# Kernel optimization log

Hardware: AMD Instinct MI355X
Metric: run time of the kernel (lower is better)

The kernel has to match this reference:

```python
import jax, jax.numpy as jnp
import numpy as np

N, E = 50000, 800000
DIM_IN, DIM_H, DIM_OUT, HEADS = 128, 16, 64, 8
NEG_SLOPE = 0.2  # PyG GATv2Conv default


def setup_inputs() -> dict:
    key = jax.random.key(0)
    ks = jax.random.split(key, 10)
    s = 0.1
    x = jax.random.normal(ks[0], (N, DIM_IN), jnp.float32)
    edge_index = jax.random.randint(ks[1], (2, E), 0, N, dtype=jnp.int32)
    Wl1 = jax.random.normal(ks[2], (DIM_IN, HEADS * DIM_H), jnp.float32) * s
    Wr1 = jax.random.normal(ks[3], (DIM_IN, HEADS * DIM_H), jnp.float32) * s
    att1 = jax.random.normal(ks[4], (HEADS, DIM_H), jnp.float32) * s
    b1 = jnp.zeros((HEADS * DIM_H,), jnp.float32)
    Wl2 = jax.random.normal(ks[5], (HEADS * DIM_H, DIM_OUT), jnp.float32) * s
    Wr2 = jax.random.normal(ks[6], (HEADS * DIM_H, DIM_OUT), jnp.float32) * s
    att2 = jax.random.normal(ks[7], (1, DIM_OUT), jnp.float32) * s
    b2 = jnp.zeros((DIM_OUT,), jnp.float32)
    return dict(x=x, edge_index=edge_index, Wl1=Wl1, Wr1=Wr1, att1=att1, b1=b1,
                Wl2=Wl2, Wr2=Wr2, att2=att2, b2=b2)


def gatv2_conv(x, src, dst, Wl, Wr, att, bias, heads, out_ch):
    # PyG GATv2Conv (share_weights=False, concat=True)
    n = x.shape[0]
    xl = (x @ Wl).reshape(n, heads, out_ch)  # source-side transform
    xr = (x @ Wr).reshape(n, heads, out_ch)  # target-side transform
    e = jax.nn.leaky_relu(xl[src] + xr[dst], NEG_SLOPE)          # [E, H, C]
    logits = jnp.einsum('ehc,hc->eh', e, att)                    # [E, H]
    # segment softmax over incoming edges of each dst node
    m = jax.lax.stop_gradient(jax.ops.segment_max(logits, dst, num_segments=n))
    ex = jnp.exp(logits - m[dst])
    denom = jax.ops.segment_sum(ex, dst, num_segments=n)
    alpha = ex / denom[dst]                                      # [E, H]
    out = jax.ops.segment_sum(xl[src] * alpha[..., None], dst, num_segments=n)
    return out.reshape(n, heads * out_ch) + bias


def reference(x, edge_index, Wl1, Wr1, att1, b1, Wl2, Wr2, att2, b2):
    n = x.shape[0]
    loops = jnp.arange(n, dtype=edge_index.dtype)
    src = jnp.concatenate([edge_index[0], loops])  # add_self_loops=True
    dst = jnp.concatenate([edge_index[1], loops])
    h = gatv2_conv(x, src, dst, Wl1, Wr1, att1, b1, HEADS, DIM_H)
    h = jax.nn.elu(h)
    out = gatv2_conv(h, src, dst, Wl2, Wr2, att2, b2, 1, DIM_OUT)
    return jax.nn.log_softmax(out, axis=1)
```

## Files before the change

kernel.cpp:

```cpp
#include <hip/hip_runtime.h>
#include <cstdint>

#define DIM_IN 128
#define HEADS 8
#define DIM_H 16
#define H1 128
#define DIM_OUT 64
#define NEG 0.2f
#define CAP 6144

typedef __attribute__((ext_vector_type(8))) short bf16x8;
typedef __attribute__((ext_vector_type(4))) float f32x4;

__device__ __forceinline__ float blo(uint32_t u) { return __uint_as_float(u << 16); }
__device__ __forceinline__ float bhi(uint32_t u) { return __uint_as_float(u & 0xffff0000u); }
__device__ __forceinline__ unsigned short f2b(float f) {
  uint32_t u = __float_as_uint(f);
  u += 0x7fffu + ((u >> 16) & 1u);
  return (unsigned short)(u >> 16);
}

#define KP 0.86561702453337804f
#define KM 0.57707801635558536f

__global__ __launch_bounds__(256) void prep_fused(
    const float* __restrict__ x, unsigned short* __restrict__ xb, int totx,
    const float* __restrict__ W0, const float* __restrict__ W1,
    const float* __restrict__ W2, const float* __restrict__ W3,
    unsigned short* __restrict__ T0, unsigned short* __restrict__ T1,
    unsigned short* __restrict__ T2, unsigned short* __restrict__ T3,
    int xblocks) {
  int bx = blockIdx.x;
  if (bx < xblocks) {
    int i = (bx * 256 + threadIdx.x) * 8;
    if (i >= totx) return;
    float4 a = *(const float4*)(x + i);
    float4 b = *(const float4*)(x + i + 4);
    ushort4 u0 = {f2b(a.x), f2b(a.y), f2b(a.z), f2b(a.w)};
    ushort4 u1 = {f2b(b.x), f2b(b.y), f2b(b.z), f2b(b.w)};
    *(ushort4*)(xb + i) = u0;
    *(ushort4*)(xb + i + 4) = u1;
  } else {
    int wz = bx - xblocks;
    int z = wz >> 6;
    const float* W = (z == 0) ? W0 : (z == 1) ? W1 : (z == 2) ? W2 : W3;
    unsigned short* T = (z == 0) ? T0 : (z == 1) ? T1 : (z == 2) ? T2 : T3;
    int M = (z < 2) ? 128 : 64;
    int t = (wz & 63) * 256 + threadIdx.x;
    if (t >= M * 128) return;
    int n = t >> 7, k = t & 127;
    T[t] = f2b(W[k * M + n]);
  }
}

template <int M>
__global__ __launch_bounds__(256) void gemm_mfma(
    const unsigned short* __restrict__ A,
    const unsigned short* __restrict__ Bt0, const unsigned short* __restrict__ Bt1,
    unsigned short* __restrict__ C0, unsigned short* __restrict__ C1, int Nrows) {
  constexpr int K = 128;
  constexpr int LDA = 72;
  constexpr int MT = M / 2;
  constexpr int NT = MT / 16;
  __shared__ __align__(16) short Asm[128 * LDA];
  __shared__ __align__(16) short Bsm[M * LDA];
  const unsigned short* __restrict__ Bt = blockIdx.z ? Bt1 : Bt0;
  unsigned short* __restrict__ Cb = blockIdx.z ? C1 : C0;
  const int row0 = blockIdx.x * 128;
  const int tid = threadIdx.x;
  const int w = tid >> 6, lane = tid & 63;
  const int l = lane & 15, q = lane >> 4;
  const int wrow = (w >> 1) * 64, wcol = (w & 1) * MT;

  f32x4 zero = {0.f, 0.f, 0.f, 0.f};
  f32x4 acc[4][NT];
#pragma unroll
  for (int ti = 0; ti < 4; ++ti)
#pragma unroll
    for (int tj = 0; tj < NT; ++tj) acc[ti][tj] = zero;

  for (int k0 = 0; k0 < K; k0 += 64) {
    __syncthreads();
    {
      int r = tid >> 1, sg = (tid & 1) * 32;
      int grow = row0 + r;
      const uint4* src = (const uint4*)(A + (size_t)grow * K + k0 + sg);
      uint4 z4 = make_uint4(0, 0, 0, 0);
#pragma unroll
      for (int i = 0; i < 4; ++i) {
        uint4 v = (grow < Nrows) ? src[i] : z4;
        *(uint4*)(Asm + r * LDA + sg + i * 8) = v;
      }
    }
    {
      int r = tid >> 1, sg = (tid & 1) * 32;
      if (r < M) {
        const uint4* src = (const uint4*)(Bt + (size_t)r * K + k0 + sg);
#pragma unroll
        for (int i = 0; i < 4; ++i)
          *(uint4*)(Bsm + r * LDA + sg + i * 8) = src[i];
      }
    }
    __syncthreads();
#pragma unroll
    for (int kk = 0; kk < 64; kk += 32) {
      bf16x8 af[4], bfr[NT];
#pragma unroll
      for (int ti = 0; ti < 4; ++ti)
        af[ti] = *(const bf16x8*)(Asm + (wrow + ti * 16 + l) * LDA + kk + q * 8);
#pragma unroll
      for (int tj = 0; tj < NT; ++tj)
        bfr[tj] = *(const bf16x8*)(Bsm + (wcol + tj * 16 + l) * LDA + kk + q * 8);
#pragma unroll
      for (int ti = 0; ti < 4; ++ti)
#pragma unroll
        for (int tj = 0; tj < NT; ++tj)
          acc[ti][tj] = __builtin_amdgcn_mfma_f32_16x16x32_bf16(
              af[ti], bfr[tj], acc[ti][tj], 0, 0, 0);
    }
  }
#pragma unroll
  for (int ti = 0; ti < 4; ++ti) {
#pragma unroll
    for (int tj = 0; tj < NT; ++tj) {
      int col = wcol + tj * 16 + l;
#pragma unroll
      for (int r = 0; r < 4; ++r) {
        int grow = row0 + wrow + ti * 16 + q * 4 + r;
        if (grow < Nrows) Cb[(size_t)grow * M + col] = f2b(acc[ti][tj][r]);
      }
    }
  }
}

__global__ __launch_bounds__(256) void p1_bucket(
    const int* __restrict__ ei, int* __restrict__ gcnt,
    uint32_t* __restrict__ gbuf, int E, int nbkt) {
  __shared__ int hist[256];
  __shared__ int base[256];
  __shared__ int cur[256];
  int tid = threadIdx.x;
  hist[tid] = 0;
  __syncthreads();
  int e0 = blockIdx.x * 8192;
  int nE = min(8192, E - e0);
  for (int i = tid; i < nE; i += 256)
    atomicAdd(&hist[ei[E + e0 + i] >> 8], 1);
  __syncthreads();
  if (tid < nbkt) {
    int h = hist[tid];
    base[tid] = h ? atomicAdd(&gcnt[tid], h) : 0;
  }
  cur[tid] = 0;
  __syncthreads();
  for (int i = tid; i < nE; i += 256) {
    int d = ei[E + e0 + i];
    int s = ei[e0 + i];
    int b = d >> 8;
    int r = atomicAdd(&cur[b], 1);
    int pos = base[b] + r;
    if (pos < CAP) gbuf[(size_t)b * CAP + pos] = ((uint32_t)d << 16) | (uint32_t)s;
  }
}

__device__ __forceinline__ int block_excl_scan256(int v, int* tmp) {
  int lane = threadIdx.x & 63, wid = threadIdx.x >> 6;
  int x = v;
#pragma unroll
  for (int o = 1; o < 64; o <<= 1) {
    int y = __shfl_up(x, o, 64);
    if (lane >= o) x += y;
  }
  if (lane == 63) tmp[wid] = x;
  __syncthreads();
  int prefix = 0;
#pragma unroll
  for (int w = 0; w < 4; ++w) if (w < wid) prefix += tmp[w];
  __syncthreads();
  return prefix + x - v;
}

__global__ __launch_bounds__(256) void p2_fused(
    const uint32_t* __restrict__ gbuf, const int* __restrict__ gcnt,
    int* __restrict__ off, int* __restrict__ srcs, int N, int nbkt) {
  __shared__ int sb[256];
  __shared__ int hist[256];
  __shared__ int cur[256];
  __shared__ int tmp[4];
  int b = blockIdx.x, tid = threadIdx.x;
  int gv = (tid < nbkt) ? gcnt[tid] : 0;
  int gex = block_excl_scan256(gv, tmp);
  sb[tid] = gex;
  hist[tid] = 0;
  __syncthreads();
  int base = sb[b];
  int cnt = min(gcnt[b], CAP);
  const uint32_t* p = gbuf + (size_t)b * CAP;
  for (int i = tid; i < cnt; i += 256)
    atomicAdd(&hist[(p[i] >> 16) & 255], 1);
  __syncthreads();
  int d = hist[tid];
  int excl = block_excl_scan256(d, tmp);
  int idx = (b << 8) + tid;
  int o = base + excl;
  if (idx <= N) off[idx] = o;
  cur[tid] = o;
  __syncthreads();
  for (int i = tid; i < cnt; i += 256) {
    uint32_t v = p[i];
    int pos = atomicAdd(&cur[(v >> 16) & 255], 1);
    srcs[pos] = (int)(v & 0xFFFFu);
  }
}

__global__ __launch_bounds__(256) void agg_l1(
    const int* __restrict__ srcs, const int* __restrict__ off,
    const unsigned short* __restrict__ xlb, const unsigned short* __restrict__ xrb,
    const float* __restrict__ att, const float* __restrict__ b1,
    unsigned short* __restrict__ hbb, int N) {
  int wid = threadIdx.x >> 6, lane = threadIdx.x & 63;
  int node = blockIdx.x * 4 + wid;
  if (node >= N) return;
  const int l4 = lane & 15;
  const int g  = lane >> 4;
  uint4 xru = *(const uint4*)(xrb + ((size_t)node << 7) + (l4 << 3));
  float r0 = blo(xru.x), r1 = bhi(xru.x), r2 = blo(xru.y), r3 = bhi(xru.y);
  float r4 = blo(xru.z), r5 = bhi(xru.z), r6 = blo(xru.w), r7 = bhi(xru.w);
  float4 a0  = *(const float4*)(att + (l4 << 3));
  float4 a1  = *(const float4*)(att + (l4 << 3) + 4);
  float c0 = KP * a0.x, c1 = KP * a0.y, c2 = KP * a0.z, c3 = KP * a0.w;
  float c4 = KP * a1.x, c5 = KP * a1.y, c6 = KP * a1.z, c7 = KP * a1.w;
  float d0 = KM * a0.x, d1 = KM * a0.y, d2 = KM * a0.z, d3 = KM * a0.w;
  float d4 = KM * a1.x, d5 = KM * a1.y, d6 = KM * a1.z, d7 = KM * a1.w;
  float acc0 = 0.f, acc1 = 0.f, acc2 = 0.f, acc3 = 0.f;
  float acc4 = 0.f, acc5 = 0.f, acc6 = 0.f, acc7 = 0.f;
  float dsum = 0.f;
  int beg = off[node];
  int M = off[node + 1] - beg + 1;
  for (int base = 0; base < M; base += 64) {
    int nk = min(64, M - base);
    int v = base + lane;
    int sv = 0;
    if (lane < nk) sv = (v == 0) ? node : srcs[beg + v - 1];
    int niter = (nk + 3) >> 2;
    for (int it = 0; it < niter; ++it) {
      int j = (it << 2) + g;
      int s = __shfl(sv, j, 64);
      uint4 xu = *(const uint4*)(xlb + ((size_t)s << 7) + (l4 << 3));
      float x0 = blo(xu.x), x1 = bhi(xu.x), x2 = blo(xu.y), x3 = bhi(xu.y);
      float x4 = blo(xu.z), x5 = bhi(xu.z), x6 = blo(xu.w), x7 = bhi(xu.w);
      float t, p;
      t = x0 + r0; p = fmaf(d0, fabsf(t), c0 * t);
      t = x1 + r1; p = fmaf(c1, t, p); p = fmaf(d1, fabsf(t), p);
      t = x2 + r2; p = fmaf(c2, t, p); p = fmaf(d2, fabsf(t), p);
      t = x3 + r3; p = fmaf(c3, t, p); p = fmaf(d3, fabsf(t), p);
      t = x4 + r4; p = fmaf(c4, t, p); p = fmaf(d4, fabsf(t), p);
      t = x5 + r5; p = fmaf(c5, t, p); p = fmaf(d5, fabsf(t), p);
      t = x6 + r6; p = fmaf(c6, t, p); p = fmaf(d6, fabsf(t), p);
      t = x7 + r7; p = fmaf(c7, t, p); p = fmaf(d7, fabsf(t), p);
      p += __shfl_xor(p, 1, 64);
      float ev = (j < nk) ? __builtin_amdgcn_exp2f(p) : 0.f;
      acc0 = fmaf(ev, x0, acc0); acc1 = fmaf(ev, x1, acc1);
      acc2 = fmaf(ev, x2, acc2); acc3 = fmaf(ev, x3, acc3);
      acc4 = fmaf(ev, x4, acc4); acc5 = fmaf(ev, x5, acc5);
      acc6 = fmaf(ev, x6, acc6); acc7 = fmaf(ev, x7, acc7);
      dsum += ev;
    }
  }
#pragma unroll
  for (int o = 16; o <= 32; o <<= 1) {
    dsum += __shfl_xor(dsum, o, 64);
    acc0 += __shfl_xor(acc0, o, 64); acc1 += __shfl_xor(acc1, o, 64);
    acc2 += __shfl_xor(acc2, o, 64); acc3 += __shfl_xor(acc3, o, 64);
    acc4 += __shfl_xor(acc4, o, 64); acc5 += __shfl_xor(acc5, o, 64);
    acc6 += __shfl_xor(acc6, o, 64); acc7 += __shfl_xor(acc7, o, 64);
  }
  if (g == 0) {
    float inv = 1.0f / dsum;
    float4 bv0 = *(const float4*)(b1 + (l4 << 3));
    float4 bv1 = *(const float4*)(b1 + (l4 << 3) + 4);
    float o0 = fmaf(acc0, inv, bv0.x), o1 = fmaf(acc1, inv, bv0.y);
    float o2 = fmaf(acc2, inv, bv0.z), o3 = fmaf(acc3, inv, bv0.w);
    float o4 = fmaf(acc4, inv, bv1.x), o5 = fmaf(acc5, inv, bv1.y);
    float o6 = fmaf(acc6, inv, bv1.z), o7 = fmaf(acc7, inv, bv1.w);
    o0 = o0 > 0.f ? o0 : expm1f(o0); o1 = o1 > 0.f ? o1 : expm1f(o1);
    o2 = o2 > 0.f ? o2 : expm1f(o2); o3 = o3 > 0.f ? o3 : expm1f(o3);
    o4 = o4 > 0.f ? o4 : expm1f(o4); o5 = o5 > 0.f ? o5 : expm1f(o5);
    o6 = o6 > 0.f ? o6 : expm1f(o6); o7 = o7 > 0.f ? o7 : expm1f(o7);
    ushort4 h0 = {f2b(o0), f2b(o1), f2b(o2), f2b(o3)};
    ushort4 h1 = {f2b(o4), f2b(o5), f2b(o6), f2b(o7)};
    unsigned short* ph = hbb + ((size_t)node << 7) + (l4 << 3);
    *(ushort4*)(ph)     = h0;
    *(ushort4*)(ph + 4) = h1;
  }
}

__global__ __launch_bounds__(256) void agg_l2(
    const int* __restrict__ srcs, const int* __restrict__ off,
    const unsigned short* __restrict__ xlb, const unsigned short* __restrict__ xrb,
    const float* __restrict__ att, const float* __restrict__ b2,
    float* __restrict__ out, int N) {
  int wid = threadIdx.x >> 6, lane = threadIdx.x & 63;
  int node = blockIdx.x * 4 + wid;
  if (node >= N) return;
  const int l3 = lane & 7;
  const int g  = lane >> 3;
  uint4 xru = *(const uint4*)(xrb + ((size_t)node << 6) + (l3 << 3));
  float r0 = blo(xru.x), r1 = bhi(xru.x), r2 = blo(xru.y), r3 = bhi(xru.y);
  float r4 = blo(xru.z), r5 = bhi(xru.z), r6 = blo(xru.w), r7 = bhi(xru.w);
  float4 a0  = *(const float4*)(att + (l3 << 3));
  float4 a1  = *(const float4*)(att + (l3 << 3) + 4);
  float c0 = KP * a0.x, c1 = KP * a0.y, c2 = KP * a0.z, c3 = KP * a0.w;
  float c4 = KP * a1.x, c5 = KP * a1.y, c6 = KP * a1.z, c7 = KP * a1.w;
  float d0 = KM * a0.x, d1 = KM * a0.y, d2 = KM * a0.z, d3 = KM * a0.w;
  float d4 = KM * a1.x, d5 = KM * a1.y, d6 = KM * a1.z, d7 = KM * a1.w;
  float acc0 = 0.f, acc1 = 0.f, acc2 = 0.f, acc3 = 0.f;
  float acc4 = 0.f, acc5 = 0.f, acc6 = 0.f, acc7 = 0.f;
  float dsum = 0.f;
  int beg = off[node];
  int M = off[node + 1] - beg + 1;
  for (int base = 0; base < M; base += 64) {
    int nk = min(64, M - base);
    int v = base + lane;
    int sv = 0;
    if (lane < nk) sv = (v == 0) ? node : srcs[beg + v - 1];
    int niter = (nk + 7) >> 3;
    for (int it = 0; it < niter; ++it) {
      int j = (it << 3) + g;
      int s = __shfl(sv, j, 64);
      uint4 xu = *(const uint4*)(xlb + ((size_t)s << 6) + (l3 << 3));
      float x0 = blo(xu.x), x1 = bhi(xu.x), x2 = blo(xu.y), x3 = bhi(xu.y);
      float x4 = blo(xu.z), x5 = bhi(xu.z), x6 = blo(xu.w), x7 = bhi(xu.w);
      float t, p;
      t = x0 + r0; p = fmaf(d0, fabsf(t), c0 * t);
      t = x1 + r1; p = fmaf(c1, t, p); p = fmaf(d1, fabsf(t), p);
      t = x2 + r2; p = fmaf(c2, t, p); p = fmaf(d2, fabsf(t), p);
      t = x3 + r3; p = fmaf(c3, t, p); p = fmaf(d3, fabsf(t), p);
      t = x4 + r4; p = fmaf(c4, t, p); p = fmaf(d4, fabsf(t), p);
      t = x5 + r5; p = fmaf(c5, t, p); p = fmaf(d5, fabsf(t), p);
      t = x6 + r6; p = fmaf(c6, t, p); p = fmaf(d6, fabsf(t), p);
      t = x7 + r7; p = fmaf(c7, t, p); p = fmaf(d7, fabsf(t), p);
      p += __shfl_xor(p, 1, 64);
      p += __shfl_xor(p, 2, 64);
      p += __shfl_xor(p, 4, 64);
      float ev = (j < nk) ? __builtin_amdgcn_exp2f(p) : 0.f;
      acc0 = fmaf(ev, x0, acc0); acc1 = fmaf(ev, x1, acc1);
      acc2 = fmaf(ev, x2, acc2); acc3 = fmaf(ev, x3, acc3);
      acc4 = fmaf(ev, x4, acc4); acc5 = fmaf(ev, x5, acc5);
      acc6 = fmaf(ev, x6, acc6); acc7 = fmaf(ev, x7, acc7);
      dsum += ev;
    }
  }
#pragma unroll
  for (int o = 8; o <= 32; o <<= 1) {
    dsum += __shfl_xor(dsum, o, 64);
    acc0 += __shfl_xor(acc0, o, 64); acc1 += __shfl_xor(acc1, o, 64);
    acc2 += __shfl_xor(acc2, o, 64); acc3 += __shfl_xor(acc3, o, 64);
    acc4 += __shfl_xor(acc4, o, 64); acc5 += __shfl_xor(acc5, o, 64);
    acc6 += __shfl_xor(acc6, o, 64); acc7 += __shfl_xor(acc7, o, 64);
  }
  float inv = 1.0f / dsum;
  float4 bv0 = *(const float4*)(b2 + (l3 << 3));
  float4 bv1 = *(const float4*)(b2 + (l3 << 3) + 4);
  float v0 = fmaf(acc0, inv, bv0.x), v1 = fmaf(acc1, inv, bv0.y);
  float v2 = fmaf(acc2, inv, bv0.z), v3 = fmaf(acc3, inv, bv0.w);
  float v4 = fmaf(acc4, inv, bv1.x), v5 = fmaf(acc5, inv, bv1.y);
  float v6 = fmaf(acc6, inv, bv1.z), v7 = fmaf(acc7, inv, bv1.w);
  float m = fmaxf(fmaxf(fmaxf(v0, v1), fmaxf(v2, v3)),
                  fmaxf(fmaxf(v4, v5), fmaxf(v6, v7)));
#pragma unroll
  for (int o = 1; o <= 4; o <<= 1) m = fmaxf(m, __shfl_xor(m, o, 64));
  float s = __expf(v0 - m) + __expf(v1 - m) + __expf(v2 - m) + __expf(v3 - m)
          + __expf(v4 - m) + __expf(v5 - m) + __expf(v6 - m) + __expf(v7 - m);
#pragma unroll
  for (int o = 1; o <= 4; o <<= 1) s += __shfl_xor(s, o, 64);
  if (g == 0) {
    float ls = __logf(s) + m;
    float* po = out + ((size_t)node << 6) + (l3 << 3);
    *(float4*)(po)     = make_float4(v0 - ls, v1 - ls, v2 - ls, v3 - ls);
    *(float4*)(po + 4) = make_float4(v4 - ls, v5 - ls, v6 - ls, v7 - ls);
  }
}

extern "C" void kernel_launch(void* const* d_in, const int* in_sizes, int n_in,
                              void* d_out, int out_size, void* d_ws, size_t ws_size,
                              hipStream_t stream) {
  const float* x    = (const float*)d_in[0];
  const int*   ei   = (const int*)d_in[1];
  const float* Wl1  = (const float*)d_in[2];
  const float* Wr1  = (const float*)d_in[3];
  const float* att1 = (const float*)d_in[4];
  const float* b1   = (const float*)d_in[5];
  const float* Wl2  = (const float*)d_in[6];
  const float* Wr2  = (const float*)d_in[7];
  const float* att2 = (const float*)d_in[8];
  const float* b2   = (const float*)d_in[9];
  float* out = (float*)d_out;

  const int N = in_sizes[0] / DIM_IN;
  const int E = in_sizes[1] / 2;
  const int nb = (N + 255) / 256;

  unsigned short* us = (unsigned short*)d_ws;
  const size_t szNH = (size_t)N * H1;
  unsigned short* xb   = us;
  unsigned short* xlb1 = xb + szNH;
  unsigned short* xrb1 = xlb1 + szNH;
  unsigned short* hbb  = xrb1 + szNH;
  unsigned short* xlb2 = hbb + szNH;
  unsigned short* xrb2 = xlb2 + (size_t)N * DIM_OUT;
  unsigned short* wt0  = xrb2 + (size_t)N * DIM_OUT;
  unsigned short* wt1  = wt0 + 16384;
  unsigned short* wt2  = wt1 + 16384;
  unsigned short* wt3  = wt2 + 8192;
  int* ibase  = (int*)(wt3 + 8192);
  int* off    = ibase;
  int* gcnt   = ibase + N + 1;
  int* srcs   = ibase + N + 1 + 256;
  uint32_t* gbuf = (uint32_t*)(srcs + E);

  hipMemsetAsync(gcnt, 0, 256 * sizeof(int), stream);
  p1_bucket<<<(E + 8191) / 8192, 256, 0, stream>>>(ei, gcnt, gbuf, E, nb);
  p2_fused<<<nb, 256, 0, stream>>>(gbuf, gcnt, off, srcs, N, nb);

  int totx = N * DIM_IN;
  int xblocks = (totx / 8 + 255) / 256;
  prep_fused<<<xblocks + 256, 256, 0, stream>>>(
      x, xb, totx, Wl1, Wr1, Wl2, Wr2, wt0, wt1, wt2, wt3, xblocks);

  const int gb = (N + 127) / 128;

  gemm_mfma<128><<<dim3(gb, 1, 2), 256, 0, stream>>>(xb, wt0, wt1, xlb1, xrb1, N);
  agg_l1<<<(N + 3) / 4, 256, 0, stream>>>(srcs, off, xlb1, xrb1, att1, b1, hbb, N);

  gemm_mfma<64><<<dim3(gb, 1, 2), 256, 0, stream>>>(hbb, wt2, wt3, xlb2, xrb2, N);
  agg_l2<<<(N + 3) / 4, 256, 0, stream>>>(srcs, off, xlb2, xrb2, att2, b2, out, N);
}
```

Before: 247.3 us.

## Software-pipeline gathered neighbor loads in GAT aggregation kernels, shrink blocks

Both aggregation kernels now process two edge groups per iteration and prefetch the next two neighbor rows before computing on the current ones, so global gather latency overlaps with the attention math. The logit dot product is split into two independent FMA chains to shorten dependency latency, and address math uses 32-bit byte offsets. Blocks shrink from 4 to 2 waves to make scheduling finer-grained. This adds register pressure and some wasted speculative loads (wrapped indices) on tail iterations.

```diff
diff --git a/kernel.cpp b/kernel.cpp
--- a/kernel.cpp
+++ b/kernel.cpp
@@ -213,13 +213,36 @@
   }
 }
 
-__global__ __launch_bounds__(256) void agg_l1(
+#define L1_BODY(XC, JV)                                                        \
+  {                                                                            \
+    float x0 = blo(XC.x), x1 = bhi(XC.x), x2 = blo(XC.y), x3 = bhi(XC.y);      \
+    float x4 = blo(XC.z), x5 = bhi(XC.z), x6 = blo(XC.w), x7 = bhi(XC.w);      \
+    float t, pa, pb;                                                           \
+    t = x0 + r0; pa = c0 * t;          pb = d0 * fabsf(t);                     \
+    t = x1 + r1; pa = fmaf(c1, t, pa); pb = fmaf(d1, fabsf(t), pb);            \
+    t = x2 + r2; pa = fmaf(c2, t, pa); pb = fmaf(d2, fabsf(t), pb);            \
+    t = x3 + r3; pa = fmaf(c3, t, pa); pb = fmaf(d3, fabsf(t), pb);            \
+    t = x4 + r4; pa = fmaf(c4, t, pa); pb = fmaf(d4, fabsf(t), pb);            \
+    t = x5 + r5; pa = fmaf(c5, t, pa); pb = fmaf(d5, fabsf(t), pb);            \
+    t = x6 + r6; pa = fmaf(c6, t, pa); pb = fmaf(d6, fabsf(t), pb);            \
+    t = x7 + r7; pa = fmaf(c7, t, pa); pb = fmaf(d7, fabsf(t), pb);            \
+    float p = pa + pb;                                                         \
+    p += __shfl_xor(p, 1, 64);                                                 \
+    float ev = ((JV) < nk) ? __builtin_amdgcn_exp2f(p) : 0.f;                  \
+    acc0 = fmaf(ev, x0, acc0); acc1 = fmaf(ev, x1, acc1);                      \
+    acc2 = fmaf(ev, x2, acc2); acc3 = fmaf(ev, x3, acc3);                      \
+    acc4 = fmaf(ev, x4, acc4); acc5 = fmaf(ev, x5, acc5);                      \
+    acc6 = fmaf(ev, x6, acc6); acc7 = fmaf(ev, x7, acc7);                      \
+    dsum += ev;                                                                \
+  }
+
+__global__ __launch_bounds__(128) void agg_l1(
     const int* __restrict__ srcs, const int* __restrict__ off,
     const unsigned short* __restrict__ xlb, const unsigned short* __restrict__ xrb,
     const float* __restrict__ att, const float* __restrict__ b1,
     unsigned short* __restrict__ hbb, int N) {
   int wid = threadIdx.x >> 6, lane = threadIdx.x & 63;
-  int node = blockIdx.x * 4 + wid;
+  int node = blockIdx.x * 2 + wid;
   if (node >= N) return;
   const int l4 = lane & 15;
   const int g  = lane >> 4;
@@ -235,6 +258,7 @@
   float acc0 = 0.f, acc1 = 0.f, acc2 = 0.f, acc3 = 0.f;
   float acc4 = 0.f, acc5 = 0.f, acc6 = 0.f, acc7 = 0.f;
   float dsum = 0.f;
+  const uint32_t lo4 = (uint32_t)(l4 << 4);
   int beg = off[node];
   int M = off[node + 1] - beg + 1;
   for (int base = 0; base < M; base += 64) {
@@ -243,28 +267,25 @@
     int sv = 0;
     if (lane < nk) sv = (v == 0) ? node : srcs[beg + v - 1];
     int niter = (nk + 3) >> 2;
-    for (int it = 0; it < niter; ++it) {
-      int j = (it << 2) + g;
-      int s = __shfl(sv, j, 64);
-      uint4 xu = *(const uint4*)(xlb + ((size_t)s << 7) + (l4 << 3));
-      float x0 = blo(xu.x), x1 = bhi(xu.x), x2 = blo(xu.y), x3 = bhi(xu.y);
-      float x4 = blo(xu.z), x5 = bhi(xu.z), x6 = blo(xu.w), x7 = bhi(xu.w);
-      float t, p;
-      t = x0 + r0; p = fmaf(d0, fabsf(t), c0 * t);
-      t = x1 + r1; p = fmaf(c1, t, p); p = fmaf(d1, fabsf(t), p);
-      t = x2 + r2; p = fmaf(c2, t, p); p = fmaf(d2, fabsf(t), p);
-      t = x3 + r3; p = fmaf(c3, t, p); p = fmaf(d3, fabsf(t), p);
-      t = x4 + r4; p = fmaf(c4, t, p); p = fmaf(d4, fabsf(t), p);
-      t = x5 + r5; p = fmaf(c5, t, p); p = fmaf(d5, fabsf(t), p);
-      t = x6 + r6; p = fmaf(c6, t, p); p = fmaf(d6, fabsf(t), p);
-      t = x7 + r7; p = fmaf(c7, t, p); p = fmaf(d7, fabsf(t), p);
-      p += __shfl_xor(p, 1, 64);
-      float ev = (j < nk) ? __builtin_amdgcn_exp2f(p) : 0.f;
-      acc0 = fmaf(ev, x0, acc0); acc1 = fmaf(ev, x1, acc1);
-      acc2 = fmaf(ev, x2, acc2); acc3 = fmaf(ev, x3, acc3);
-      acc4 = fmaf(ev, x4, acc4); acc5 = fmaf(ev, x5, acc5);
-      acc6 = fmaf(ev, x6, acc6); acc7 = fmaf(ev, x7, acc7);
-      dsum += ev;
+    int sA = __shfl(sv, g, 64);
+    uint4 xA = *(const uint4*)((const char*)xlb + (((uint32_t)sA << 8) | lo4));
+    int sB = __shfl(sv, (4 + g) & 63, 64);
+    uint4 xB = *(const uint4*)((const char*)xlb + (((uint32_t)sB << 8) | lo4));
+    int it = 0;
+    for (; it + 1 < niter; it += 2) {
+      int jA = (it << 2) + g;
+      int jB = jA + 4;
+      int sA2 = __shfl(sv, (jA + 8) & 63, 64);
+      int sB2 = __shfl(sv, (jB + 8) & 63, 64);
+      uint4 nA = *(const uint4*)((const char*)xlb + (((uint32_t)sA2 << 8) | lo4));
+      uint4 nB = *(const uint4*)((const char*)xlb + (((uint32_t)sB2 << 8) | lo4));
+      L1_BODY(xA, jA)
+      L1_BODY(xB, jB)
+      xA = nA; xB = nB;
+    }
+    if (it < niter) {
+      int jA = (it << 2) + g;
+      L1_BODY(xA, jA)
     }
   }
 #pragma unroll
@@ -295,13 +316,38 @@
   }
 }
 
-__global__ __launch_bounds__(256) void agg_l2(
+#define L2_BODY(XC, JV)                                                        \
+  {                                                                            \
+    float x0 = blo(XC.x), x1 = bhi(XC.x), x2 = blo(XC.y), x3 = bhi(XC.y);      \
+    float x4 = blo(XC.z), x5 = bhi(XC.z), x6 = blo(XC.w), x7 = bhi(XC.w);      \
+    float t, pa, pb;                                                           \
+    t = x0 + r0; pa = c0 * t;          pb = d0 * fabsf(t);                     \
+    t = x1 + r1; pa = fmaf(c1, t, pa); pb = fmaf(d1, fabsf(t), pb);            \
+    t = x2 + r2; pa = fmaf(c2, t, pa); pb = fmaf(d2, fabsf(t), pb);            \
+    t = x3 + r3; pa = fmaf(c3, t, pa); pb = fmaf(d3, fabsf(t), pb);            \
+    t = x4 + r4; pa = fmaf(c4, t, pa); pb = fmaf(d4, fabsf(t), pb);            \
+    t = x5 + r5; pa = fmaf(c5, t, pa); pb = fmaf(d5, fabsf(t), pb);            \
+    t = x6 + r6; pa = fmaf(c6, t, pa); pb = fmaf(d6, fabsf(t), pb);            \
+    t = x7 + r7; pa = fmaf(c7, t, pa); pb = fmaf(d7, fabsf(t), pb);            \
+    float p = pa + pb;                                                         \
+    p += __shfl_xor(p, 1, 64);                                                 \
+    p += __shfl_xor(p, 2, 64);                                                 \
+    p += __shfl_xor(p, 4, 64);                                                 \
+    float ev = ((JV) < nk) ? __builtin_amdgcn_exp2f(p) : 0.f;                  \
+    acc0 = fmaf(ev, x0, acc0); acc1 = fmaf(ev, x1, acc1);                      \
+    acc2 = fmaf(ev, x2, acc2); acc3 = fmaf(ev, x3, acc3);                      \
+    acc4 = fmaf(ev, x4, acc4); acc5 = fmaf(ev, x5, acc5);                      \
+    acc6 = fmaf(ev, x6, acc6); acc7 = fmaf(ev, x7, acc7);                      \
+    dsum += ev;                                                                \
+  }
+
+__global__ __launch_bounds__(128) void agg_l2(
     const int* __restrict__ srcs, const int* __restrict__ off,
     const unsigned short* __restrict__ xlb, const unsigned short* __restrict__ xrb,
     const float* __restrict__ att, const float* __restrict__ b2,
     float* __restrict__ out, int N) {
   int wid = threadIdx.x >> 6, lane = threadIdx.x & 63;
-  int node = blockIdx.x * 4 + wid;
+  int node = blockIdx.x * 2 + wid;
   if (node >= N) return;
   const int l3 = lane & 7;
   const int g  = lane >> 3;
@@ -317,6 +363,7 @@
   float acc0 = 0.f, acc1 = 0.f, acc2 = 0.f, acc3 = 0.f;
   float acc4 = 0.f, acc5 = 0.f, acc6 = 0.f, acc7 = 0.f;
   float dsum = 0.f;
+  const uint32_t lo3 = (uint32_t)(l3 << 4);
   int beg = off[node];
   int M = off[node + 1] - beg + 1;
   for (int base = 0; base < M; base += 64) {
@@ -325,30 +372,25 @@
     int sv = 0;
     if (lane < nk) sv = (v == 0) ? node : srcs[beg + v - 1];
     int niter = (nk + 7) >> 3;
-    for (int it = 0; it < niter; ++it) {
-      int j = (it << 3) + g;
-      int s = __shfl(sv, j, 64);
-      uint4 xu = *(const uint4*)(xlb + ((size_t)s << 6) + (l3 << 3));
-      float x0 = blo(xu.x), x1 = bhi(xu.x), x2 = blo(xu.y), x3 = bhi(xu.y);
-      float x4 = blo(xu.z), x5 = bhi(xu.z), x6 = blo(xu.w), x7 = bhi(xu.w);
-      float t, p;
-      t = x0 + r0; p = fmaf(d0, fabsf(t), c0 * t);
-      t = x1 + r1; p = fmaf(c1, t, p); p = fmaf(d1, fabsf(t), p);
-      t = x2 + r2; p = fmaf(c2, t, p); p = fmaf(d2, fabsf(t), p);
-      t = x3 + r3; p = fmaf(c3, t, p); p = fmaf(d3, fabsf(t), p);
-      t = x4 + r4; p = fmaf(c4, t, p); p = fmaf(d4, fabsf(t), p);
-      t = x5 + r5; p = fmaf(c5, t, p); p = fmaf(d5, fabsf(t), p);
-      t = x6 + r6; p = fmaf(c6, t, p); p = fmaf(d6, fabsf(t), p);
-      t = x7 + r7; p = fmaf(c7, t, p); p = fmaf(d7, fabsf(t), p);
-      p += __shfl_xor(p, 1, 64);
-      p += __shfl_xor(p, 2, 64);
-      p += __shfl_xor(p, 4, 64);
-      float ev = (j < nk) ? __builtin_amdgcn_exp2f(p) : 0.f;
-      acc0 = fmaf(ev, x0, acc0); acc1 = fmaf(ev, x1, acc1);
-      acc2 = fmaf(ev, x2, acc2); acc3 = fmaf(ev, x3, acc3);
-      acc4 = fmaf(ev, x4, acc4); acc5 = fmaf(ev, x5, acc5);
-      acc6 = fmaf(ev, x6, acc6); acc7 = fmaf(ev, x7, acc7);
-      dsum += ev;
+    int sA = __shfl(sv, g, 64);
+    uint4 xA = *(const uint4*)((const char*)xlb + (((uint32_t)sA << 7) | lo3));
+    int sB = __shfl(sv, (8 + g) & 63, 64);
+    uint4 xB = *(const uint4*)((const char*)xlb + (((uint32_t)sB << 7) | lo3));
+    int it = 0;
+    for (; it + 1 < niter; it += 2) {
+      int jA = (it << 3) + g;
+      int jB = jA + 8;
+      int sA2 = __shfl(sv, (jA + 16) & 63, 64);
+      int sB2 = __shfl(sv, (jB + 16) & 63, 64);
+      uint4 nA = *(const uint4*)((const char*)xlb + (((uint32_t)sA2 << 7) | lo3));
+      uint4 nB = *(const uint4*)((const char*)xlb + (((uint32_t)sB2 << 7) | lo3));
+      L2_BODY(xA, jA)
+      L2_BODY(xB, jB)
+      xA = nA; xB = nB;
+    }
+    if (it < niter) {
+      int jA = (it << 3) + g;
+      L2_BODY(xA, jA)
     }
   }
 #pragma unroll
@@ -431,8 +473,8 @@
   const int gb = (N + 127) / 128;
 
   gemm_mfma<128><<<dim3(gb, 1, 2), 256, 0, stream>>>(xb, wt0, wt1, xlb1, xrb1, N);
-  agg_l1<<<(N + 3) / 4, 256, 0, stream>>>(srcs, off, xlb1, xrb1, att1, b1, hbb, N);
+  agg_l1<<<(N + 1) / 2, 128, 0, stream>>>(srcs, off, xlb1, xrb1, att1, b1, hbb, N);
 
   gemm_mfma<64><<<dim3(gb, 1, 2), 256, 0, stream>>>(hbb, wt2, wt3, xlb2, xrb2, N);
-  agg_l2<<<(N + 3) / 4, 256, 0, stream>>>(srcs, off, xlb2, xrb2, att2, b2, out, N);
-}
+  agg_l2<<<(N + 1) / 2, 128, 0, stream>>>(srcs, off, xlb2, xrb2, att2, b2, out, N);
+}
```

Result: no change. 252.0 us (+1.9%).
